# Kernel tuning notes

Hardware: AMD Instinct MI355X
Metric: run time of the kernel (lower is better)

Reference implementation:

```python
import jax, jax.numpy as jnp
import numpy as np

WS = 7; SHIFT = 3; HEADS = 4; DIM = 192; C2 = 2 * DIM; HD = C2 // HEADS
H = W = 60
PAD = (WS - H % WS) % WS          # 3
HP = H + PAD; WP = W + PAD        # 63
NW = (HP // WS) * (WP // WS)      # 81 windows
N = WS * WS                       # 49 tokens per window
MLP_H = int(4.0 * C2)             # 1536


def _rel_pos_index():
    coords = np.stack(np.meshgrid(np.arange(WS), np.arange(WS), indexing='ij'))
    cf = coords.reshape(2, -1)
    rel = (cf[:, :, None] - cf[:, None, :]).transpose(1, 2, 0)
    rel[:, :, 0] += WS - 1
    rel[:, :, 1] += WS - 1
    rel[:, :, 0] *= 2 * WS - 1
    return rel.sum(-1)  # (N, N) into table of size (2*WS-1)^2


def _attn_mask():
    img = np.zeros((HP, WP))
    cnt = 0
    for hs in (slice(0, -WS), slice(-WS, -SHIFT), slice(-SHIFT, None)):
        for ws_ in (slice(0, -WS), slice(-WS, -SHIFT), slice(-SHIFT, None)):
            img[hs, ws_] = cnt; cnt += 1
    mw = img.reshape(HP // WS, WS, WP // WS, WS).transpose(0, 2, 1, 3).reshape(-1, N)
    diff = mw[:, None, :] - mw[:, :, None]
    return np.where(diff != 0, -100.0, 0.0).astype(np.float32)  # (NW, N, N)

REL_IDX = jnp.asarray(_rel_pos_index().reshape(-1))
ATTN_MASK = jnp.asarray(_attn_mask())


def layernorm(x, w, b, eps=1e-5):
    mu = jnp.mean(x, axis=-1, keepdims=True)
    var = jnp.var(x, axis=-1, keepdims=True)
    return (x - mu) * jax.lax.rsqrt(var + eps) * w + b


def setup_inputs() -> dict:
    key = jax.random.key(0)
    ks = jax.random.split(key, 16)
    s = 0.02
    return {
        'x': jax.random.normal(ks[0], (8, DIM, H, W), jnp.float32),
        'g': jax.random.normal(ks[1], (8, DIM, H, W), jnp.float32),
        'norm_w': jnp.ones((C2,), jnp.float32),
        'norm_b': jnp.zeros((C2,), jnp.float32),
        'n1_w': jnp.ones((C2,), jnp.float32),
        'n1_b': jnp.zeros((C2,), jnp.float32),
        'qkv_w': jax.random.normal(ks[2], (3 * C2, C2), jnp.float32) * s,
        'qkv_b': jnp.zeros((3 * C2,), jnp.float32),
        'proj_w': jax.random.normal(ks[3], (C2, C2), jnp.float32) * s,
        'proj_b': jnp.zeros((C2,), jnp.float32),
        'rpb': jax.random.normal(ks[4], ((2 * WS - 1) ** 2, HEADS), jnp.float32) * s,
        'n2_w': jnp.ones((C2,), jnp.float32),
        'n2_b': jnp.zeros((C2,), jnp.float32),
        'fc1_w': jax.random.normal(ks[5], (MLP_H, C2), jnp.float32) * s,
        'fc1_b': jnp.zeros((MLP_H,), jnp.float32),
        'fc2_w': jax.random.normal(ks[6], (C2, MLP_H), jnp.float32) * s,
        'fc2_b': jnp.zeros((C2,), jnp.float32),
        'conv_w': jax.random.normal(ks[7], (DIM, C2, 3, 3), jnp.float32) * s,
        'conv_b': jnp.zeros((DIM,), jnp.float32),
    }


def reference(x, g, norm_w, norm_b, n1_w, n1_b, qkv_w, qkv_b, proj_w, proj_b,
              rpb, n2_w, n2_b, fc1_w, fc1_b, fc2_w, fc2_b, conv_w, conv_b):
    B = x.shape[0]
    # concat + NCHW -> NHWC + pad to window multiple
    comb = jnp.concatenate([x, g], axis=1).transpose(0, 2, 3, 1)   # (B,H,W,2C)
    comb = jnp.pad(comb, ((0, 0), (0, PAD), (0, PAD), (0, 0)))     # (B,HP,WP,2C)
    z = layernorm(comb, norm_w, norm_b)
    # ---- Swin block ----
    shortcut = z
    zn = layernorm(z, n1_w, n1_b)
    zn = jnp.roll(zn, shift=(-SHIFT, -SHIFT), axis=(1, 2))
    # window partition -> (B*NW, N, 2C)
    w = zn.reshape(B, HP // WS, WS, WP // WS, WS, C2).transpose(0, 1, 3, 2, 4, 5)
    w = w.reshape(B * NW, N, C2)
    qkv = (w @ qkv_w.T + qkv_b).reshape(B * NW, N, 3, HEADS, HD).transpose(2, 0, 3, 1, 4)
    q, k, v = qkv[0], qkv[1], qkv[2]                               # (B*NW,H,N,HD)
    attn = jnp.einsum('bhnd,bhmd->bhnm', q, k) * (HD ** -0.5)
    bias = rpb[REL_IDX].reshape(N, N, HEADS).transpose(2, 0, 1)    # (H,N,N)
    attn = attn + bias[None]
    attn = attn.reshape(B, NW, HEADS, N, N) + ATTN_MASK[None, :, None]
    attn = jax.nn.softmax(attn.reshape(B * NW, HEADS, N, N), axis=-1)
    out = jnp.einsum('bhnm,bhmd->bhnd', attn, v).transpose(0, 2, 1, 3).reshape(B * NW, N, C2)
    out = out @ proj_w.T + proj_b
    # window reverse + unshift
    out = out.reshape(B, HP // WS, WP // WS, WS, WS, C2).transpose(0, 1, 3, 2, 4, 5)
    out = out.reshape(B, HP, WP, C2)
    out = jnp.roll(out, shift=(SHIFT, SHIFT), axis=(1, 2))
    z = shortcut + out
    h = layernorm(z, n2_w, n2_b)
    h = jax.nn.gelu(h @ fc1_w.T + fc1_b, approximate=False)
    z = z + (h @ fc2_w.T + fc2_b)
    # crop, NHWC -> NCHW, 3x3 reduce conv, residual
    z = z[:, :H, :W, :].transpose(0, 3, 1, 2)                      # (B,2C,H,W)
    red = jax.lax.conv_general_dilated(
        z, conv_w, window_strides=(1, 1), padding=((1, 1), (1, 1)),
        dimension_numbers=('NCHW', 'OIHW', 'NCHW')) + conv_b[None, :, None, None]
    return red + x
```

## Files before the change

kernel.cpp:

```cpp
#include <hip/hip_runtime.h>
#include <cstddef>
#include <cstdint>

#define HEADS   4
#define C2c     384
#define HPc     63
#define WPc     63
#define NWc     81
#define BATCH   8
#define TOKP    (BATCH*HPc*WPc)
#define TOKC    (BATCH*60*60)
#define MLPH    1536
#define TPB     3969
#define CONVK   3456
#define CONVN   192

typedef __attribute__((ext_vector_type(8))) short short8;
typedef __attribute__((ext_vector_type(4))) float f32x4;
typedef unsigned short u16;

__device__ __forceinline__ u16 f2bf(float f) {
  unsigned u = __float_as_uint(f);
  u += 0x7fff + ((u >> 16) & 1);
  return (u16)(u >> 16);
}
__device__ __forceinline__ float bf2f(u16 b) { return __uint_as_float((unsigned)b << 16); }

#define GLOAD16(gp, lp) __builtin_amdgcn_global_load_lds( \
    (const __attribute__((address_space(1))) unsigned*)(gp), \
    (__attribute__((address_space(3))) unsigned*)(lp), 16, 0, 0)

__device__ __forceinline__ int xcd_swizzle(int orig, int nwg) {
  int q = nwg >> 3, r = nwg & 7;
  int xcd = orig & 7, off = orig >> 3;
  return (xcd < r ? xcd*(q+1) : r*(q+1) + (xcd - r)*q) + off;
}

__device__ __forceinline__ float2 block_reduce_384(float v, float* red) {
  __syncthreads();
  float s = v, q = v * v;
  #pragma unroll
  for (int o = 32; o > 0; o >>= 1) {
    s += __shfl_down(s, o);
    q += __shfl_down(q, o);
  }
  int w = threadIdx.x >> 6;
  if ((threadIdx.x & 63) == 0) { red[2*w] = s; red[2*w+1] = q; }
  __syncthreads();
  float ts = red[0]+red[2]+red[4]+red[6]+red[8]+red[10];
  float tq = red[1]+red[3]+red[5]+red[7]+red[9]+red[11];
  return make_float2(ts, tq);
}

__global__ __launch_bounds__(384)
void k1a_kernel(const float* __restrict__ x, const float* __restrict__ g,
                const float* __restrict__ nw, const float* __restrict__ nb,
                const float* __restrict__ n1w, const float* __restrict__ n1b,
                float* __restrict__ musig, u16* __restrict__ wbuf)
{
  __shared__ float red[12];
  int t = blockIdx.x;
  int b = t / (HPc*WPc);
  int rem = t - b*(HPc*WPc);
  int i = rem / WPc, j = rem - (rem / WPc)*WPc;
  int c = threadIdx.x;

  float v = 0.f;
  if (i < 60 && j < 60) {
    if (c < 192) v = x[(((size_t)b*192 + c)*60 + i)*60 + j];
    else         v = g[(((size_t)b*192 + (c-192))*60 + i)*60 + j];
  }
  float2 ss = block_reduce_384(v, red);
  float mu  = ss.x * (1.f/384.f);
  float var = ss.y * (1.f/384.f) - mu*mu;
  float rs  = rsqrtf(var + 1e-5f);
  if (c == 0) { musig[2*t] = mu; musig[2*t+1] = rs; }
  float zi  = (v - mu) * rs * nw[c] + nb[c];
  float2 s2 = block_reduce_384(zi, red);
  float mu2  = s2.x * (1.f/384.f);
  float var2 = s2.y * (1.f/384.f) - mu2*mu2;
  float zn = (zi - mu2) * rsqrtf(var2 + 1e-5f) * n1w[c] + n1b[c];
  int ai = i - 3; if (ai < 0) ai += HPc;
  int aj = j - 3; if (aj < 0) aj += WPc;
  int win = (ai/7)*9 + (aj/7);
  int tok = (ai%7)*7 + (aj%7);
  wbuf[(((size_t)b*NWc + win)*49 + tok)*C2c + c] = f2bf(zn);
}

__global__ __launch_bounds__(384)
void k1b_kernel(const float* __restrict__ x, const float* __restrict__ g,
                const float* __restrict__ nw, const float* __restrict__ nb,
                const float* __restrict__ musig, float* __restrict__ z)
{
  int tc = blockIdx.x;
  int b = tc / 3600;
  int rem = tc - b*3600;
  int i = rem / 60, j = rem - (rem/60)*60;
  int t = b*(HPc*WPc) + i*WPc + j;
  int c = threadIdx.x;
  float v;
  if (c < 192) v = x[(((size_t)b*192 + c)*60 + i)*60 + j];
  else         v = g[(((size_t)b*192 + (c-192))*60 + i)*60 + j];
  float mu = musig[2*t], rs = musig[2*t+1];
  z[(size_t)tc*C2c + c] = (v - mu) * rs * nw[c] + nb[c];
}

__global__ __launch_bounds__(384)
void ln2_kernel(const float* __restrict__ z, const float* __restrict__ nw,
                const float* __restrict__ nb, u16* __restrict__ out)
{
  __shared__ float red[12];
  int tc = blockIdx.x;
  int c = threadIdx.x;
  float v = z[(size_t)tc*C2c + c];
  float2 ss = block_reduce_384(v, red);
  float mu  = ss.x * (1.f/384.f);
  float var = ss.y * (1.f/384.f) - mu*mu;
  out[(size_t)tc*C2c + c] = f2bf((v - mu) * rsqrtf(var + 1e-5f) * nw[c] + nb[c]);
}

__global__ __launch_bounds__(256)
void f2bf_kernel(const float* __restrict__ in, u16* __restrict__ out, int n4)
{
  int t = blockIdx.x*256 + threadIdx.x;
  if (t >= n4) return;
  float4 v = ((const float4*)in)[t];
  ushort4 o;
  o.x = f2bf(v.x); o.y = f2bf(v.y); o.z = f2bf(v.z); o.w = f2bf(v.w);
  ((ushort4*)out)[t] = o;
}

__global__ void split_convw(const float* __restrict__ cw, u16* __restrict__ hi, u16* __restrict__ lo)
{
  int t = blockIdx.x*blockDim.x + threadIdx.x;
  if (t >= CONVN*CONVK) return;
  int oc = t / CONVK, k = t - oc*CONVK;
  int p = k / 384, c = k - p*384;
  float v = cw[((size_t)oc*384 + c)*9 + p];
  u16 h = f2bf(v);
  hi[t] = h;
  lo[t] = f2bf(v - bf2f(h));
}

template<int EPI>
__global__ __launch_bounds__(256)
void mfma_gemm(const u16* __restrict__ A, const u16* __restrict__ B,
               const float* __restrict__ bias, u16* __restrict__ Cb, float* __restrict__ zbuf,
               int M, int N, int K, int ldb, int addbias)
{
  __shared__ u16 As [128*64];
  __shared__ u16 Bs [128*64];
  int tid = threadIdx.x;
  int lane = tid & 63, w = tid >> 6;
  int wr = w >> 1, wc = w & 1;
  int nwg = gridDim.x * gridDim.y;
  int swz = xcd_swizzle(blockIdx.y*gridDim.x + blockIdx.x, nwg);
  int bx = swz % gridDim.x, by = swz / gridDim.x;
  int m0 = by * 128, n0 = bx * 128;
  int srow = lane >> 3, sslot = (lane & 7) ^ srow;

  f32x4 acc[4][4];
  #pragma unroll
  for (int i = 0; i < 4; ++i)
    #pragma unroll
    for (int j = 0; j < 4; ++j) acc[i][j] = (f32x4){0.f,0.f,0.f,0.f};

  char* AsB = (char*)As; char* BsB = (char*)Bs;
  int r15 = lane & 15, kq = lane >> 4;

  for (int k0 = 0; k0 < K; k0 += 64) {
    #pragma unroll
    for (int i = 0; i < 4; ++i) {
      int rblk = w*4 + i;
      int ar = m0 + rblk*8 + srow; if (ar >= M) ar = M - 1;
      int br = n0 + rblk*8 + srow;
      GLOAD16(A + (size_t)ar*K   + k0 + sslot*8, AsB + rblk*1024);
      GLOAD16(B + (size_t)br*ldb + k0 + sslot*8, BsB + rblk*1024);
    }
    __syncthreads();
    #pragma unroll
    for (int ks = 0; ks < 2; ++ks) {
      int slog = ks*4 + kq;
      short8 af[4], bf[4];
      #pragma unroll
      for (int mi = 0; mi < 4; ++mi) {
        int row = wr*64 + mi*16 + r15;
        af[mi] = *(const short8*)(AsB + row*128 + ((slog ^ (row&7))<<4));
      }
      #pragma unroll
      for (int ni = 0; ni < 4; ++ni) {
        int row = wc*64 + ni*16 + r15;
        bf[ni] = *(const short8*)(BsB + row*128 + ((slog ^ (row&7))<<4));
      }
      #pragma unroll
      for (int mi = 0; mi < 4; ++mi)
        #pragma unroll
        for (int ni = 0; ni < 4; ++ni)
          acc[mi][ni] = __builtin_amdgcn_mfma_f32_16x16x32_bf16(af[mi], bf[ni], acc[mi][ni], 0, 0, 0);
    }
    __syncthreads();
  }

  int fq = lane >> 4, fr = lane & 15;
  #pragma unroll
  for (int mi = 0; mi < 4; ++mi) {
    #pragma unroll
    for (int j = 0; j < 4; ++j) {
      int m = m0 + wr*64 + mi*16 + fq*4 + j;
      if (m >= M) continue;
      int zrow = 0; bool zok = true;
      if (EPI == 1) {
        int b = m / TPB;
        int rem = m - b*TPB;
        int win = rem / 49, tok = rem - (rem/49)*49;
        int wh = win/9, ww = win - (win/9)*9;
        int th = tok/7, tw = tok - (tok/7)*7;
        int oi = wh*7 + th + 3; if (oi >= HPc) oi -= HPc;
        int oj = ww*7 + tw + 3; if (oj >= WPc) oj -= WPc;
        zok = (oi < 60 && oj < 60);
        zrow = (b*60 + oi)*60 + oj;
      }
      #pragma unroll
      for (int ni = 0; ni < 4; ++ni) {
        int n = n0 + wc*64 + ni*16 + fr;
        float val = acc[mi][ni][j];
        if (EPI == 0) {
          Cb[(size_t)m*N + n] = f2bf(val + bias[n]);
        } else if (EPI == 1) {
          if (zok) zbuf[(size_t)zrow*C2c + n] += val + bias[n];
        } else if (EPI == 2) {
          float vv = val + bias[n];
          float ge = 0.5f*vv*(1.f + erff(vv*0.70710678118654752f));
          Cb[(size_t)m*N + n] = f2bf(ge);
        } else if (EPI == 3) {
          float vv = val + (addbias ? bias[n] : 0.f);
          zbuf[(size_t)m*C2c + n] += vv;
        } else {
          float vv = val + (addbias ? bias[n] : 0.f) + zbuf[(size_t)m*C2c + n];
          zbuf[(size_t)m*C2c + n] = vv;
          Cb[(size_t)m*C2c + n] = f2bf(vv);
        }
      }
    }
  }
}

__global__ __launch_bounds__(256)
void mfma_conv(const u16* __restrict__ Y, const u16* __restrict__ Bh, const u16* __restrict__ Bl,
               const float* __restrict__ cb, const float* __restrict__ xres, float* __restrict__ outp)
{
  __shared__ u16 As [64*64];
  __shared__ u16 Bsh[64*64];
  __shared__ u16 Bsl[64*64];
  int tid = threadIdx.x;
  int lane = tid & 63, w = tid >> 6;
  int wr = w >> 1, wc = w & 1;
  int nwg = gridDim.x * gridDim.y;
  int swz = xcd_swizzle(blockIdx.y*gridDim.x + blockIdx.x, nwg);
  int bx = swz % 3, by = swz / 3;
  int m0 = by * 64, n0 = bx * 64;
  int srow = lane >> 3, sslot = (lane & 7) ^ srow;

  f32x4 acc[2][2];
  #pragma unroll
  for (int i = 0; i < 2; ++i)
    #pragma unroll
    for (int j = 0; j < 2; ++j) acc[i][j] = (f32x4){0.f,0.f,0.f,0.f};

  int rowA[2], pbA[2], ohA[2], owA[2];
  #pragma unroll
  for (int i = 0; i < 2; ++i) {
    int idx = i*256 + tid;
    rowA[i] = idx >> 3;
    int pix = m0 + rowA[i];
    int pb = pix / 3600;
    int prem = pix - pb*3600;
    pbA[i] = pb; ohA[i] = prem / 60; owA[i] = prem - (prem/60)*60;
  }

  char* AsB = (char*)As; char* BhB = (char*)Bsh; char* BlB = (char*)Bsl;
  int r15 = lane & 15, kq = lane >> 4;

  for (int k0 = 0; k0 < CONVK; k0 += 64) {
    int p  = k0 / 384;
    int c0 = k0 - p*384;
    int dh = p/3 - 1, dw = (p - (p/3)*3) - 1;
    #pragma unroll
    for (int i = 0; i < 2; ++i) {
      int rblk = w*2 + i;
      int br = n0 + rblk*8 + srow;
      GLOAD16(Bh + (size_t)br*CONVK + k0 + sslot*8, BhB + rblk*1024);
      GLOAD16(Bl + (size_t)br*CONVK + k0 + sslot*8, BlB + rblk*1024);
    }
    #pragma unroll
    for (int i = 0; i < 2; ++i) {
      int idx = i*256 + tid;
      int row = rowA[i], slot = idx & 7;
      int ih = ohA[i] + dh, iw = owA[i] + dw;
      int4 v = {0,0,0,0};
      if ((unsigned)ih < 60u && (unsigned)iw < 60u)
        v = *(const int4*)(Y + (size_t)(pbA[i]*3600 + ih*60 + iw)*C2c + c0 + slot*8);
      *(int4*)(AsB + row*128 + ((slot ^ (row&7))<<4)) = v;
    }
    __syncthreads();
    #pragma unroll
    for (int ks = 0; ks < 2; ++ks) {
      int slog = ks*4 + kq;
      short8 af[2], bh[2], bl[2];
      #pragma unroll
      for (int mi = 0; mi < 2; ++mi) {
        int row = wr*32 + mi*16 + r15;
        af[mi] = *(const short8*)(AsB + row*128 + ((slog ^ (row&7))<<4));
      }
      #pragma unroll
      for (int ni = 0; ni < 2; ++ni) {
        int row = wc*32 + ni*16 + r15;
        int off = row*128 + ((slog ^ (row&7))<<4);
        bh[ni] = *(const short8*)(BhB + off);
        bl[ni] = *(const short8*)(BlB + off);
      }
      #pragma unroll
      for (int mi = 0; mi < 2; ++mi)
        #pragma unroll
        for (int ni = 0; ni < 2; ++ni) {
          acc[mi][ni] = __builtin_amdgcn_mfma_f32_16x16x32_bf16(af[mi], bh[ni], acc[mi][ni], 0, 0, 0);
          acc[mi][ni] = __builtin_amdgcn_mfma_f32_16x16x32_bf16(af[mi], bl[ni], acc[mi][ni], 0, 0, 0);
        }
    }
    __syncthreads();
  }

  int fq = lane >> 4, fr = lane & 15;
  #pragma unroll
  for (int mi = 0; mi < 2; ++mi) {
    #pragma unroll
    for (int j = 0; j < 4; ++j) {
      int m = m0 + wr*32 + mi*16 + fq*4 + j;
      int pb = m / 3600;
      int rem = m - pb*3600;
      int oh = rem / 60, ow = rem - (rem/60)*60;
      #pragma unroll
      for (int ni = 0; ni < 2; ++ni) {
        int oc = n0 + wc*32 + ni*16 + fr;
        size_t oi = ((size_t)pb*192 + oc)*3600 + oh*60 + ow;
        outp[oi] = acc[mi][ni][j] + cb[oc] + xres[oi];
      }
    }
  }
}

#define QS_STRIDE 100
#define VS_STRIDE 104
#define SS_STRIDE 53

__global__ __launch_bounds__(256)
void attn_kernel(const u16* __restrict__ qkv, const float* __restrict__ rpb,
                 u16* __restrict__ out)
{
  __shared__ float qs[52*QS_STRIDE];
  __shared__ float ks[52*QS_STRIDE];
  __shared__ float S[52*SS_STRIDE];
  int blk = blockIdx.x;
  int h   = blk & 3;
  int bw  = blk >> 2;
  int win = bw % NWc;
  const u16* base = qkv + (size_t)bw*49*1152;
  int tid = threadIdx.x;

  for (int t2 = tid; t2 < 588; t2 += 256) {
    int r = t2 / 12, dq = t2 - (t2/12)*12;
    short8 qv = *(const short8*)(base + r*1152 +       h*96 + dq*8);
    short8 kv = *(const short8*)(base + r*1152 + 384 + h*96 + dq*8);
    #pragma unroll
    for (int e = 0; e < 8; ++e) {
      qs[r*QS_STRIDE + dq*8 + e] = bf2f((u16)qv[e]);
      ks[r*QS_STRIDE + dq*8 + e] = bf2f((u16)kv[e]);
    }
  }
  __syncthreads();

  const float scale = 0.1020620726159657f;
  int wh = win / 9, ww = win - (win/9)*9;

  if (tid < 169) {
    int tr = tid / 13, tc = tid - (tid/13)*13;
    int r0 = tr*4, c0 = tc*4;
    float a[4][4] = {};
    for (int k0 = 0; k0 < 96; k0 += 4) {
      float4 qv[4], kv4[4];
      #pragma unroll
      for (int i = 0; i < 4; ++i) qv[i]  = *(const float4*)&qs[(r0+i)*QS_STRIDE + k0];
      #pragma unroll
      for (int j = 0; j < 4; ++j) kv4[j] = *(const float4*)&ks[(c0+j)*QS_STRIDE + k0];
      #pragma unroll
      for (int i = 0; i < 4; ++i)
        #pragma unroll
        for (int j = 0; j < 4; ++j)
          a[i][j] += qv[i].x*kv4[j].x + qv[i].y*kv4[j].y + qv[i].z*kv4[j].z + qv[i].w*kv4[j].w;
    }
    #pragma unroll
    for (int i = 0; i < 4; ++i) {
      int r = r0 + i;
      if (r < 49) {
        int r1 = r/7, c1 = r - (r/7)*7;
        int hp1 = wh*7 + r1, wp1 = ww*7 + c1;
        int g1 = (hp1 < 56 ? 0 : (hp1 < 60 ? 1 : 2))*3 + (wp1 < 56 ? 0 : (wp1 < 60 ? 1 : 2));
        #pragma unroll
        for (int j = 0; j < 4; ++j) {
          int c = c0 + j;
          if (c < 49) {
            int r2 = c/7, c2 = c - (c/7)*7;
            float s = a[i][j]*scale + rpb[((r1 - r2 + 6)*13 + (c1 - c2 + 6))*HEADS + h];
            int hp2 = wh*7 + r2, wp2 = ww*7 + c2;
            int g2 = (hp2 < 56 ? 0 : (hp2 < 60 ? 1 : 2))*3 + (wp2 < 56 ? 0 : (wp2 < 60 ? 1 : 2));
            if (g1 != g2) s -= 100.f;
            S[r*SS_STRIDE + c] = s;
          }
        }
      }
    }
  }
  __syncthreads();

  for (int t2 = tid; t2 < 588; t2 += 256) {
    int r = t2 / 12, dq = t2 - (t2/12)*12;
    short8 vv = *(const short8*)(base + r*1152 + 768 + h*96 + dq*8);
    #pragma unroll
    for (int e = 0; e < 8; ++e) ks[r*VS_STRIDE + dq*8 + e] = bf2f((u16)vv[e]);
  }
  if (tid < 49) {
    float mx = -1e30f;
    for (int c = 0; c < 49; ++c) mx = fmaxf(mx, S[tid*SS_STRIDE + c]);
    float sum = 0.f;
    for (int c = 0; c < 49; ++c) { float e = expf(S[tid*SS_STRIDE + c] - mx); S[tid*SS_STRIDE + c] = e; sum += e; }
    float inv = 1.f / sum;
    for (int c = 0; c < 49; ++c) S[tid*SS_STRIDE + c] *= inv;
  }
  __syncthreads();

  if (tid < 156) {
    int tr2 = tid / 12, tc2 = tid - (tid/12)*12;
    int r0 = tr2*4, d0 = tc2*8;
    float o[4][8] = {};
    for (int c = 0; c < 49; ++c) {
      float4 v0 = *(const float4*)&ks[c*VS_STRIDE + d0];
      float4 v1 = *(const float4*)&ks[c*VS_STRIDE + d0 + 4];
      #pragma unroll
      for (int i = 0; i < 4; ++i) {
        float sv = S[(r0+i)*SS_STRIDE + c];
        o[i][0] += sv*v0.x; o[i][1] += sv*v0.y; o[i][2] += sv*v0.z; o[i][3] += sv*v0.w;
        o[i][4] += sv*v1.x; o[i][5] += sv*v1.y; o[i][6] += sv*v1.z; o[i][7] += sv*v1.w;
      }
    }
    #pragma unroll
    for (int i = 0; i < 4; ++i) {
      int r = r0 + i;
      if (r >= 49) continue;
      ushort4 w0, w1;
      w0.x = f2bf(o[i][0]); w0.y = f2bf(o[i][1]); w0.z = f2bf(o[i][2]); w0.w = f2bf(o[i][3]);
      w1.x = f2bf(o[i][4]); w1.y = f2bf(o[i][5]); w1.z = f2bf(o[i][6]); w1.w = f2bf(o[i][7]);
      size_t ob = ((size_t)bw*49 + r)*C2c + h*96 + d0;
      *(ushort4*)&out[ob]     = w0;
      *(ushort4*)&out[ob + 4] = w1;
    }
  }
}

extern "C" void kernel_launch(void* const* d_in, const int* in_sizes, int n_in,
                              void* d_out, int out_size, void* d_ws, size_t ws_size,
                              hipStream_t stream)
{
  const float* x      = (const float*)d_in[0];
  const float* g      = (const float*)d_in[1];
  const float* norm_w = (const float*)d_in[2];
  const float* norm_b = (const float*)d_in[3];
  const float* n1_w   = (const float*)d_in[4];
  const float* n1_b   = (const float*)d_in[5];
  const float* qkv_w  = (const float*)d_in[6];
  const float* qkv_b  = (const float*)d_in[7];
  const float* proj_w = (const float*)d_in[8];
  const float* proj_b = (const float*)d_in[9];
  const float* rpb    = (const float*)d_in[10];
  const float* n2_w   = (const float*)d_in[11];
  const float* n2_b   = (const float*)d_in[12];
  const float* fc1_w  = (const float*)d_in[13];
  const float* fc1_b  = (const float*)d_in[14];
  const float* fc2_w  = (const float*)d_in[15];
  const float* fc2_b  = (const float*)d_in[16];
  const float* conv_w = (const float*)d_in[17];
  const float* conv_b = (const float*)d_in[18];
  float* outp = (float*)d_out;

  char* p = (char*)d_ws;
  u16* wbuf = (u16*)p;              p += (size_t)TOKP*C2c*2;
  char* qr  = p;                    p += (size_t)TOKP*1152*2;
  u16*   qkvb = (u16*)qr;
  float* z    = (float*)qr;
  u16*   hid_c = (u16*)(qr + (size_t)TOKC*C2c*4);
  u16* qkvw = (u16*)p; p += 442368*2;
  u16* pw   = (u16*)p; p += 147456*2;
  u16* f1w  = (u16*)p; p += 589824*2;
  u16* f2w  = (u16*)p; p += 589824*2;
  u16* cvwh = (u16*)p; p += (size_t)CONVN*CONVK*2;
  u16* cvwl = (u16*)p; p += (size_t)CONVN*CONVK*2;
  float* musig = (float*)p; p += (size_t)TOKP*2*4;
  u16* hid_f = (u16*)p;
  size_t need_full = (size_t)(p - (char*)d_ws) + (size_t)TOKC*MLPH*2;
  bool full_mlp = ws_size >= need_full;

  f2bf_kernel<<<(442368/4 + 255)/256, 256, 0, stream>>>(qkv_w, qkvw, 442368/4);
  f2bf_kernel<<<(147456/4 + 255)/256, 256, 0, stream>>>(proj_w, pw, 147456/4);
  f2bf_kernel<<<(589824/4 + 255)/256, 256, 0, stream>>>(fc1_w, f1w, 589824/4);
  f2bf_kernel<<<(589824/4 + 255)/256, 256, 0, stream>>>(fc2_w, f2w, 589824/4);
  split_convw<<<(CONVN*CONVK + 255)/256, 256, 0, stream>>>(conv_w, cvwh, cvwl);

  k1a_kernel<<<TOKP, 384, 0, stream>>>(x, g, norm_w, norm_b, n1_w, n1_b, musig, wbuf);

  mfma_gemm<0><<<dim3(9, 249), 256, 0, stream>>>(
      wbuf, qkvw, qkv_b, qkvb, nullptr, TOKP, 1152, 384, 384, 1);

  attn_kernel<<<BATCH*NWc*HEADS, 256, 0, stream>>>(qkvb, rpb, wbuf);

  k1b_kernel<<<TOKC, 384, 0, stream>>>(x, g, norm_w, norm_b, musig, z);

  mfma_gemm<1><<<dim3(3, 249), 256, 0, stream>>>(
      wbuf, pw, proj_b, nullptr, z, TOKP, 384, 384, 384, 1);

  ln2_kernel<<<TOKC, 384, 0, stream>>>(z, n2_w, n2_b, wbuf);

  if (full_mlp) {
    mfma_gemm<2><<<dim3(12, 225), 256, 0, stream>>>(
        wbuf, f1w, fc1_b, hid_f, nullptr, TOKC, MLPH, 384, 384, 1);
    mfma_gemm<4><<<dim3(3, 225), 256, 0, stream>>>(
        hid_f, f2w, fc2_b, wbuf, z, TOKC, 384, MLPH, MLPH, 1);
  } else {
    for (int h0 = 0; h0 < MLPH; h0 += 384) {
      mfma_gemm<2><<<dim3(3, 225), 256, 0, stream>>>(
          wbuf, f1w + (size_t)h0*384, fc1_b + h0,
          hid_c, nullptr, TOKC, 384, 384, 384, 1);
      if (h0 < MLPH - 384)
        mfma_gemm<3><<<dim3(3, 225), 256, 0, stream>>>(
            hid_c, f2w + h0, fc2_b,
            nullptr, z, TOKC, 384, 384, MLPH, h0 == 0 ? 1 : 0);
      else
        mfma_gemm<4><<<dim3(3, 225), 256, 0, stream>>>(
            hid_c, f2w + h0, fc2_b,
            wbuf, z, TOKC, 384, 384, MLPH, 0);
    }
  }

  mfma_conv<<<dim3(3, 450), 256, 0, stream>>>(wbuf, cvwh, cvwl, conv_b, x, outp);
}
```

Baseline: 747.3 us.

## Widen conv K-tile to 128 with async loads and chunk the fallback MLP by rows

```diff
diff --git a/kernel.cpp b/kernel.cpp
--- a/kernel.cpp
+++ b/kernel.cpp
@@ -129,6 +129,8 @@
   o.x = f2bf(v.x); o.y = f2bf(v.y); o.z = f2bf(v.z); o.w = f2bf(v.w);
   ((ushort4*)out)[t] = o;
 }
+
+__global__ void zero_kernel(uint4* p) { p[threadIdx.x] = make_uint4(0,0,0,0); }
 
 __global__ void split_convw(const float* __restrict__ cw, u16* __restrict__ hi, u16* __restrict__ lo)
 {
@@ -247,11 +249,12 @@
 
 __global__ __launch_bounds__(256)
 void mfma_conv(const u16* __restrict__ Y, const u16* __restrict__ Bh, const u16* __restrict__ Bl,
-               const float* __restrict__ cb, const float* __restrict__ xres, float* __restrict__ outp)
-{
-  __shared__ u16 As [64*64];
-  __shared__ u16 Bsh[64*64];
-  __shared__ u16 Bsl[64*64];
+               const float* __restrict__ cb, const float* __restrict__ xres,
+               const u16* __restrict__ zpad, float* __restrict__ outp)
+{
+  __shared__ u16 As [64*128];
+  __shared__ u16 Bsh[64*128];
+  __shared__ u16 Bsl[64*128];
   int tid = threadIdx.x;
   int lane = tid & 63, w = tid >> 6;
   int wr = w >> 1, wc = w & 1;
@@ -259,7 +262,7 @@
   int swz = xcd_swizzle(blockIdx.y*gridDim.x + blockIdx.x, nwg);
   int bx = swz % 3, by = swz / 3;
   int m0 = by * 64, n0 = bx * 64;
-  int srow = lane >> 3, sslot = (lane & 7) ^ srow;
+  int l4 = lane >> 4;
 
   f32x4 acc[2][2];
   #pragma unroll
@@ -267,55 +270,60 @@
     #pragma unroll
     for (int j = 0; j < 2; ++j) acc[i][j] = (f32x4){0.f,0.f,0.f,0.f};
 
-  int rowA[2], pbA[2], ohA[2], owA[2];
-  #pragma unroll
-  for (int i = 0; i < 2; ++i) {
-    int idx = i*256 + tid;
-    rowA[i] = idx >> 3;
-    int pix = m0 + rowA[i];
+  int pbA[4], ohA[4], owA[4], ssA[4], cA[4];
+  #pragma unroll
+  for (int i = 0; i < 4; ++i) {
+    cA[i] = i*4 + w;
+    int row = cA[i]*4 + l4;
+    int pix = m0 + row;
     int pb = pix / 3600;
     int prem = pix - pb*3600;
     pbA[i] = pb; ohA[i] = prem / 60; owA[i] = prem - (prem/60)*60;
+    ssA[i] = (lane & 15) ^ (row & 7);
+  }
+  int brB[4], ssB[4], cB[4];
+  #pragma unroll
+  for (int j = 0; j < 4; ++j) {
+    cB[j] = j*4 + w;
+    int row = cB[j]*4 + l4;
+    brB[j] = n0 + row;
+    ssB[j] = (lane & 15) ^ (row & 7);
   }
 
   char* AsB = (char*)As; char* BhB = (char*)Bsh; char* BlB = (char*)Bsl;
   int r15 = lane & 15, kq = lane >> 4;
 
-  for (int k0 = 0; k0 < CONVK; k0 += 64) {
+  for (int k0 = 0; k0 < CONVK; k0 += 128) {
     int p  = k0 / 384;
     int c0 = k0 - p*384;
     int dh = p/3 - 1, dw = (p - (p/3)*3) - 1;
     #pragma unroll
-    for (int i = 0; i < 2; ++i) {
-      int rblk = w*2 + i;
-      int br = n0 + rblk*8 + srow;
-      GLOAD16(Bh + (size_t)br*CONVK + k0 + sslot*8, BhB + rblk*1024);
-      GLOAD16(Bl + (size_t)br*CONVK + k0 + sslot*8, BlB + rblk*1024);
-    }
-    #pragma unroll
-    for (int i = 0; i < 2; ++i) {
-      int idx = i*256 + tid;
-      int row = rowA[i], slot = idx & 7;
+    for (int j = 0; j < 4; ++j) {
+      GLOAD16(Bh + (size_t)brB[j]*CONVK + k0 + ssB[j]*8, BhB + cB[j]*1024);
+      GLOAD16(Bl + (size_t)brB[j]*CONVK + k0 + ssB[j]*8, BlB + cB[j]*1024);
+    }
+    #pragma unroll
+    for (int i = 0; i < 4; ++i) {
       int ih = ohA[i] + dh, iw = owA[i] + dw;
-      int4 v = {0,0,0,0};
-      if ((unsigned)ih < 60u && (unsigned)iw < 60u)
-        v = *(const int4*)(Y + (size_t)(pbA[i]*3600 + ih*60 + iw)*C2c + c0 + slot*8);
-      *(int4*)(AsB + row*128 + ((slot ^ (row&7))<<4)) = v;
+      const u16* src = ((unsigned)ih < 60u && (unsigned)iw < 60u)
+        ? Y + ((size_t)pbA[i]*3600 + ih*60 + iw)*C2c + c0 + ssA[i]*8
+        : zpad;
+      GLOAD16(src, AsB + cA[i]*1024);
     }
     __syncthreads();
     #pragma unroll
-    for (int ks = 0; ks < 2; ++ks) {
+    for (int ks = 0; ks < 4; ++ks) {
       int slog = ks*4 + kq;
       short8 af[2], bh[2], bl[2];
       #pragma unroll
       for (int mi = 0; mi < 2; ++mi) {
         int row = wr*32 + mi*16 + r15;
-        af[mi] = *(const short8*)(AsB + row*128 + ((slog ^ (row&7))<<4));
+        af[mi] = *(const short8*)(AsB + row*256 + ((slog ^ (row&7))<<4));
       }
       #pragma unroll
       for (int ni = 0; ni < 2; ++ni) {
         int row = wc*32 + ni*16 + r15;
-        int off = row*128 + ((slog ^ (row&7))<<4);
+        int off = row*256 + ((slog ^ (row&7))<<4);
         bh[ni] = *(const short8*)(BhB + off);
         bl[ni] = *(const short8*)(BlB + off);
       }
@@ -504,6 +512,7 @@
   u16* cvwh = (u16*)p; p += (size_t)CONVN*CONVK*2;
   u16* cvwl = (u16*)p; p += (size_t)CONVN*CONVK*2;
   float* musig = (float*)p; p += (size_t)TOKP*2*4;
+  u16* zpad = (u16*)p; p += 256;
   u16* hid_f = (u16*)p;
   size_t need_full = (size_t)(p - (char*)d_ws) + (size_t)TOKC*MLPH*2;
   bool full_mlp = ws_size >= need_full;
@@ -513,6 +522,7 @@
   f2bf_kernel<<<(589824/4 + 255)/256, 256, 0, stream>>>(fc1_w, f1w, 589824/4);
   f2bf_kernel<<<(589824/4 + 255)/256, 256, 0, stream>>>(fc2_w, f2w, 589824/4);
   split_convw<<<(CONVN*CONVK + 255)/256, 256, 0, stream>>>(conv_w, cvwh, cvwl);
+  zero_kernel<<<1, 16, 0, stream>>>((uint4*)zpad);
 
   k1a_kernel<<<TOKP, 384, 0, stream>>>(x, g, norm_w, norm_b, n1_w, n1_b, musig, wbuf);
 
@@ -534,20 +544,14 @@
     mfma_gemm<4><<<dim3(3, 225), 256, 0, stream>>>(
         hid_f, f2w, fc2_b, wbuf, z, TOKC, 384, MLPH, MLPH, 1);
   } else {
-    for (int h0 = 0; h0 < MLPH; h0 += 384) {
-      mfma_gemm<2><<<dim3(3, 225), 256, 0, stream>>>(
-          wbuf, f1w + (size_t)h0*384, fc1_b + h0,
-          hid_c, nullptr, TOKC, 384, 384, 384, 1);
-      if (h0 < MLPH - 384)
-        mfma_gemm<3><<<dim3(3, 225), 256, 0, stream>>>(
-            hid_c, f2w + h0, fc2_b,
-            nullptr, z, TOKC, 384, 384, MLPH, h0 == 0 ? 1 : 0);
-      else
-        mfma_gemm<4><<<dim3(3, 225), 256, 0, stream>>>(
-            hid_c, f2w + h0, fc2_b,
-            wbuf, z, TOKC, 384, 384, MLPH, 0);
-    }
-  }
-
-  mfma_conv<<<dim3(3, 450), 256, 0, stream>>>(wbuf, cvwh, cvwl, conv_b, x, outp);
-}
+    const int CH = 9600;
+    for (int off = 0; off < TOKC; off += CH) {
+      mfma_gemm<2><<<dim3(12, 75), 256, 0, stream>>>(
+          wbuf + (size_t)off*C2c, f1w, fc1_b, hid_c, nullptr, CH, MLPH, 384, 384, 1);
+      mfma_gemm<4><<<dim3(3, 75), 256, 0, stream>>>(
+          hid_c, f2w, fc2_b, wbuf + (size_t)off*C2c, z + (size_t)off*C2c, CH, 384, MLPH, MLPH, 1);
+    }
+  }
+
+  mfma_conv<<<dim3(3, 450), 256, 0, stream>>>(wbuf, cvwh, cvwl, conv_b, x, zpad, outp);
+}
```

After: 745.4 us. No clear change (-0.2%).

## Fuse shortcut LayerNorm into proj epilogue and async-load conv A tiles

Applied to the files above, without the earlier changes.

```diff
diff --git a/kernel.cpp b/kernel.cpp
--- a/kernel.cpp
+++ b/kernel.cpp
@@ -88,24 +88,6 @@
 }
 
 __global__ __launch_bounds__(384)
-void k1b_kernel(const float* __restrict__ x, const float* __restrict__ g,
-                const float* __restrict__ nw, const float* __restrict__ nb,
-                const float* __restrict__ musig, float* __restrict__ z)
-{
-  int tc = blockIdx.x;
-  int b = tc / 3600;
-  int rem = tc - b*3600;
-  int i = rem / 60, j = rem - (rem/60)*60;
-  int t = b*(HPc*WPc) + i*WPc + j;
-  int c = threadIdx.x;
-  float v;
-  if (c < 192) v = x[(((size_t)b*192 + c)*60 + i)*60 + j];
-  else         v = g[(((size_t)b*192 + (c-192))*60 + i)*60 + j];
-  float mu = musig[2*t], rs = musig[2*t+1];
-  z[(size_t)tc*C2c + c] = (v - mu) * rs * nw[c] + nb[c];
-}
-
-__global__ __launch_bounds__(384)
 void ln2_kernel(const float* __restrict__ z, const float* __restrict__ nw,
                 const float* __restrict__ nb, u16* __restrict__ out)
 {
@@ -130,6 +112,8 @@
   ((ushort4*)out)[t] = o;
 }
 
+__global__ void zero_kernel(uint4* p) { p[threadIdx.x] = make_uint4(0,0,0,0); }
+
 __global__ void split_convw(const float* __restrict__ cw, u16* __restrict__ hi, u16* __restrict__ lo)
 {
   int t = blockIdx.x*blockDim.x + threadIdx.x;
@@ -146,7 +130,10 @@
 __global__ __launch_bounds__(256)
 void mfma_gemm(const u16* __restrict__ A, const u16* __restrict__ B,
                const float* __restrict__ bias, u16* __restrict__ Cb, float* __restrict__ zbuf,
-               int M, int N, int K, int ldb, int addbias)
+               int M, int N, int K, int ldb, int addbias,
+               const float* __restrict__ xp, const float* __restrict__ gp,
+               const float* __restrict__ nw, const float* __restrict__ nb,
+               const float* __restrict__ musig)
 {
   __shared__ u16 As [128*64];
   __shared__ u16 Bs [128*64];
@@ -208,17 +195,22 @@
     for (int j = 0; j < 4; ++j) {
       int m = m0 + wr*64 + mi*16 + fq*4 + j;
       if (m >= M) continue;
-      int zrow = 0; bool zok = true;
+      int zrow = 0, b = 0, oi = 0, oj = 0; bool zok = true;
+      float mu = 0.f, rs = 0.f;
       if (EPI == 1) {
-        int b = m / TPB;
+        b = m / TPB;
         int rem = m - b*TPB;
         int win = rem / 49, tok = rem - (rem/49)*49;
         int wh = win/9, ww = win - (win/9)*9;
         int th = tok/7, tw = tok - (tok/7)*7;
-        int oi = wh*7 + th + 3; if (oi >= HPc) oi -= HPc;
-        int oj = ww*7 + tw + 3; if (oj >= WPc) oj -= WPc;
+        oi = wh*7 + th + 3; if (oi >= HPc) oi -= HPc;
+        oj = ww*7 + tw + 3; if (oj >= WPc) oj -= WPc;
         zok = (oi < 60 && oj < 60);
-        zrow = (b*60 + oi)*60 + oj;
+        if (zok) {
+          zrow = (b*60 + oi)*60 + oj;
+          int t = b*(HPc*WPc) + oi*WPc + oj;
+          mu = musig[2*t]; rs = musig[2*t+1];
+        }
       }
       #pragma unroll
       for (int ni = 0; ni < 4; ++ni) {
@@ -227,7 +219,12 @@
         if (EPI == 0) {
           Cb[(size_t)m*N + n] = f2bf(val + bias[n]);
         } else if (EPI == 1) {
-          if (zok) zbuf[(size_t)zrow*C2c + n] += val + bias[n];
+          if (zok) {
+            float xg = (n < 192) ? xp[(((size_t)b*192 + n)*60 + oi)*60 + oj]
+                                 : gp[(((size_t)b*192 + (n-192))*60 + oi)*60 + oj];
+            float ln1 = (xg - mu) * rs * nw[n] + nb[n];
+            zbuf[(size_t)zrow*C2c + n] = ln1 + val + bias[n];
+          }
         } else if (EPI == 2) {
           float vv = val + bias[n];
           float ge = 0.5f*vv*(1.f + erff(vv*0.70710678118654752f));
@@ -247,7 +244,8 @@
 
 __global__ __launch_bounds__(256)
 void mfma_conv(const u16* __restrict__ Y, const u16* __restrict__ Bh, const u16* __restrict__ Bl,
-               const float* __restrict__ cb, const float* __restrict__ xres, float* __restrict__ outp)
+               const float* __restrict__ cb, const float* __restrict__ xres,
+               const u16* __restrict__ zpad, float* __restrict__ outp)
 {
   __shared__ u16 As [64*64];
   __shared__ u16 Bsh[64*64];
@@ -267,15 +265,21 @@
     #pragma unroll
     for (int j = 0; j < 2; ++j) acc[i][j] = (f32x4){0.f,0.f,0.f,0.f};
 
-  int rowA[2], pbA[2], ohA[2], owA[2];
+  int pbA[2], ohA[2], owA[2], cA[2];
   #pragma unroll
   for (int i = 0; i < 2; ++i) {
-    int idx = i*256 + tid;
-    rowA[i] = idx >> 3;
-    int pix = m0 + rowA[i];
+    cA[i] = w*2 + i;
+    int row = cA[i]*8 + srow;
+    int pix = m0 + row;
     int pb = pix / 3600;
     int prem = pix - pb*3600;
     pbA[i] = pb; ohA[i] = prem / 60; owA[i] = prem - (prem/60)*60;
+  }
+  int brB[2], cB[2];
+  #pragma unroll
+  for (int j = 0; j < 2; ++j) {
+    cB[j] = w*2 + j;
+    brB[j] = n0 + cB[j]*8 + srow;
   }
 
   char* AsB = (char*)As; char* BhB = (char*)Bsh; char* BlB = (char*)Bsl;
@@ -286,21 +290,17 @@
     int c0 = k0 - p*384;
     int dh = p/3 - 1, dw = (p - (p/3)*3) - 1;
     #pragma unroll
+    for (int j = 0; j < 2; ++j) {
+      GLOAD16(Bh + (size_t)brB[j]*CONVK + k0 + sslot*8, BhB + cB[j]*1024);
+      GLOAD16(Bl + (size_t)brB[j]*CONVK + k0 + sslot*8, BlB + cB[j]*1024);
+    }
+    #pragma unroll
     for (int i = 0; i < 2; ++i) {
-      int rblk = w*2 + i;
-      int br = n0 + rblk*8 + srow;
-      GLOAD16(Bh + (size_t)br*CONVK + k0 + sslot*8, BhB + rblk*1024);
-      GLOAD16(Bl + (size_t)br*CONVK + k0 + sslot*8, BlB + rblk*1024);
-    }
-    #pragma unroll
-    for (int i = 0; i < 2; ++i) {
-      int idx = i*256 + tid;
-      int row = rowA[i], slot = idx & 7;
       int ih = ohA[i] + dh, iw = owA[i] + dw;
-      int4 v = {0,0,0,0};
-      if ((unsigned)ih < 60u && (unsigned)iw < 60u)
-        v = *(const int4*)(Y + (size_t)(pbA[i]*3600 + ih*60 + iw)*C2c + c0 + slot*8);
-      *(int4*)(AsB + row*128 + ((slot ^ (row&7))<<4)) = v;
+      const u16* src = ((unsigned)ih < 60u && (unsigned)iw < 60u)
+        ? Y + ((size_t)pbA[i]*3600 + ih*60 + iw)*C2c + c0 + sslot*8
+        : zpad;
+      GLOAD16(src, AsB + cA[i]*1024);
     }
     __syncthreads();
     #pragma unroll
@@ -492,11 +492,6 @@
   float* outp = (float*)d_out;
 
   char* p = (char*)d_ws;
-  u16* wbuf = (u16*)p;              p += (size_t)TOKP*C2c*2;
-  char* qr  = p;                    p += (size_t)TOKP*1152*2;
-  u16*   qkvb = (u16*)qr;
-  float* z    = (float*)qr;
-  u16*   hid_c = (u16*)(qr + (size_t)TOKC*C2c*4);
   u16* qkvw = (u16*)p; p += 442368*2;
   u16* pw   = (u16*)p; p += 147456*2;
   u16* f1w  = (u16*)p; p += 589824*2;
@@ -504,8 +499,13 @@
   u16* cvwh = (u16*)p; p += (size_t)CONVN*CONVK*2;
   u16* cvwl = (u16*)p; p += (size_t)CONVN*CONVK*2;
   float* musig = (float*)p; p += (size_t)TOKP*2*4;
-  u16* hid_f = (u16*)p;
-  size_t need_full = (size_t)(p - (char*)d_ws) + (size_t)TOKC*MLPH*2;
+  u16* zpad = (u16*)p; p += 256;
+  u16* wbuf = (u16*)p; p += (size_t)TOKP*C2c*2;
+  char* qr  = p;       p += (size_t)TOKP*1152*2;
+  u16*   qkvb = (u16*)qr;
+  float* z    = (float*)qr;
+  u16*   hid  = (u16*)(qr + (size_t)TOKC*C2c*4);
+  size_t need_full = (size_t)((char*)hid - (char*)d_ws) + (size_t)TOKC*MLPH*2;
   bool full_mlp = ws_size >= need_full;
 
   f2bf_kernel<<<(442368/4 + 255)/256, 256, 0, stream>>>(qkv_w, qkvw, 442368/4);
@@ -513,41 +513,44 @@
   f2bf_kernel<<<(589824/4 + 255)/256, 256, 0, stream>>>(fc1_w, f1w, 589824/4);
   f2bf_kernel<<<(589824/4 + 255)/256, 256, 0, stream>>>(fc2_w, f2w, 589824/4);
   split_convw<<<(CONVN*CONVK + 255)/256, 256, 0, stream>>>(conv_w, cvwh, cvwl);
+  zero_kernel<<<1, 16, 0, stream>>>((uint4*)zpad);
 
   k1a_kernel<<<TOKP, 384, 0, stream>>>(x, g, norm_w, norm_b, n1_w, n1_b, musig, wbuf);
 
   mfma_gemm<0><<<dim3(9, 249), 256, 0, stream>>>(
-      wbuf, qkvw, qkv_b, qkvb, nullptr, TOKP, 1152, 384, 384, 1);
+      wbuf, qkvw, qkv_b, qkvb, nullptr, TOKP, 1152, 384, 384, 1,
+      nullptr, nullptr, nullptr, nullptr, nullptr);
 
   attn_kernel<<<BATCH*NWc*HEADS, 256, 0, stream>>>(qkvb, rpb, wbuf);
 
-  k1b_kernel<<<TOKC, 384, 0, stream>>>(x, g, norm_w, norm_b, musig, z);
-
   mfma_gemm<1><<<dim3(3, 249), 256, 0, stream>>>(
-      wbuf, pw, proj_b, nullptr, z, TOKP, 384, 384, 384, 1);
+      wbuf, pw, proj_b, nullptr, z, TOKP, 384, 384, 384, 1,
+      x, g, norm_w, norm_b, musig);
 
   ln2_kernel<<<TOKC, 384, 0, stream>>>(z, n2_w, n2_b, wbuf);
 
   if (full_mlp) {
     mfma_gemm<2><<<dim3(12, 225), 256, 0, stream>>>(
-        wbuf, f1w, fc1_b, hid_f, nullptr, TOKC, MLPH, 384, 384, 1);
+        wbuf, f1w, fc1_b, hid, nullptr, TOKC, MLPH, 384, 384, 1,
+        nullptr, nullptr, nullptr, nullptr, nullptr);
     mfma_gemm<4><<<dim3(3, 225), 256, 0, stream>>>(
-        hid_f, f2w, fc2_b, wbuf, z, TOKC, 384, MLPH, MLPH, 1);
+        hid, f2w, fc2_b, wbuf, z, TOKC, 384, MLPH, MLPH, 1,
+        nullptr, nullptr, nullptr, nullptr, nullptr);
   } else {
     for (int h0 = 0; h0 < MLPH; h0 += 384) {
       mfma_gemm<2><<<dim3(3, 225), 256, 0, stream>>>(
-          wbuf, f1w + (size_t)h0*384, fc1_b + h0,
-          hid_c, nullptr, TOKC, 384, 384, 384, 1);
+          wbuf, f1w + (size_t)h0*384, fc1_b + h0, hid, nullptr, TOKC, 384, 384, 384, 1,
+          nullptr, nullptr, nullptr, nullptr, nullptr);
       if (h0 < MLPH - 384)
         mfma_gemm<3><<<dim3(3, 225), 256, 0, stream>>>(
-            hid_c, f2w + h0, fc2_b,
-            nullptr, z, TOKC, 384, 384, MLPH, h0 == 0 ? 1 : 0);
+            hid, f2w + h0, fc2_b, nullptr, z, TOKC, 384, 384, MLPH, h0 == 0 ? 1 : 0,
+            nullptr, nullptr, nullptr, nullptr, nullptr);
       else
         mfma_gemm<4><<<dim3(3, 225), 256, 0, stream>>>(
-            hid_c, f2w + h0, fc2_b,
-            wbuf, z, TOKC, 384, 384, MLPH, 0);
-    }
-  }
-
-  mfma_conv<<<dim3(3, 450), 256, 0, stream>>>(wbuf, cvwh, cvwl, conv_b, x, outp);
-}
+            hid, f2w + h0, fc2_b, wbuf, z, TOKC, 384, 384, MLPH, 0,
+            nullptr, nullptr, nullptr, nullptr, nullptr);
+    }
+  }
+
+  mfma_conv<<<dim3(3, 450), 256, 0, stream>>>(wbuf, cvwh, cvwl, conv_b, x, zpad, outp);
+}
```

Result: slower. 786.6 us (+5.3%).
